# Optimization experiments

Hardware: AMD Instinct MI355X
Metric: run time of the kernel (lower is better)

## Reference

```python
import jax, jax.numpy as jnp
import numpy as np

B_SZ, T_LEN, M_DIM, S_DIM = 128, 8192, 64, 512
EPS = 1e-16  # stands in for config.R_epsilon / E_epsilon / l_epsilon


def setup_inputs() -> dict:
    key = jax.random.key(0)
    k1, k2, k3 = jax.random.split(key, 3)
    # one-hot encoded higher-order emission symbols, as the model feeds the cell
    sym = jax.random.randint(k1, (B_SZ, T_LEN), 0, M_DIM)
    x = jax.nn.one_hot(sym, M_DIM, dtype=jnp.float32)          # [B, T, M]
    # row-stochastic transition matrix (model.A(A_kernel) produces probabilities)
    A = jax.nn.softmax(jax.random.normal(k2, (S_DIM, S_DIM)), axis=1)
    # emission matrix: column s is the emission distribution of state s
    B = jax.nn.softmax(jax.random.normal(k3, (M_DIM, S_DIM)), axis=0)
    return {"x": x, "A": A, "B": B}


def _logsumexp_row(alpha):
    # calc_new_cell_state: log(sum(exp(alpha - m) + l_eps)) + m, over states
    m = jnp.max(alpha, axis=1, keepdims=True)
    return jnp.log(jnp.sum(jnp.exp(alpha - m) + EPS, axis=1, keepdims=True)) + m


def reference(x, A, B):
    bsz, T, M = x.shape
    S = A.shape[0]
    # E_t = x_t @ B for all t at once (same math as per-step get_E)
    E = jnp.einsum('btm,ms->bts', x, B)                         # [B, T, S]

    # get_initial_state: all probability mass on state 0
    init_fwd = jnp.concatenate(
        [jnp.ones((bsz, 1), x.dtype), jnp.zeros((bsz, S - 1), x.dtype)], axis=1)
    # first call has init=True: R = log(old_forward)
    R0 = jnp.log(init_fwd)                                      # [0, -inf, ...]
    alpha0 = jnp.log(E[:, 0] + EPS) + R0                        # [B, S]

    def step(alpha_prev, E_t):
        # get_R: max-subtract log-domain sparse/dense matmul trick
        m = jnp.max(alpha_prev, axis=1, keepdims=True)
        R = jnp.log(jnp.exp(alpha_prev - m) @ A + EPS) + m
        # calc_new_cell_state
        alpha = jnp.log(E_t + EPS) + R
        return alpha, None

    E_time_major = jnp.swapaxes(E, 0, 1)                        # [T, B, S]
    alpha_T, _ = jax.lax.scan(step, alpha0, E_time_major[1:])
    loglik = _logsumexp_row(alpha_T)                            # [B, 1]
    return alpha_T, loglik
```

## Files before the change

kernel.cpp:

```cpp
#include <hip/hip_runtime.h>
#include <stdint.h>

#define BSZ  128
#define TLEN 8192
#define MDIM 64
#define SDIM 512
#define NEG_BIG (-1e30f)
#define QA   127

typedef int i32x4 __attribute__((ext_vector_type(4)));

__device__ __forceinline__ float wave_max_f32(float x) {
  int v = __builtin_bit_cast(int, x);
#define DPP_STEP(ctrl)                                                        \
  {                                                                           \
    int o = __builtin_amdgcn_update_dpp(v, v, ctrl, 0xf, 0xf, false);         \
    v = __builtin_bit_cast(int, fmaxf(__builtin_bit_cast(float, v),           \
                                      __builtin_bit_cast(float, o)));         \
  }
  DPP_STEP(0x111)
  DPP_STEP(0x112)
  DPP_STEP(0x114)
  DPP_STEP(0x118)
  DPP_STEP(0x142)
  DPP_STEP(0x143)
#undef DPP_STEP
  return __builtin_bit_cast(float, __builtin_amdgcn_readlane(v, 63));
}

__global__ void sym_kernel(const float* __restrict__ x, uint8_t* __restrict__ sym) {
  int i = blockIdx.x * blockDim.x + threadIdx.x;
  const float4* p = (const float4*)(x + (size_t)i * MDIM);
  int idx = 0;
  #pragma unroll
  for (int j = 0; j < 16; ++j) {
    float4 v = p[j];
    if (v.x > 0.5f) idx = 4*j + 0;
    if (v.y > 0.5f) idx = 4*j + 1;
    if (v.z > 0.5f) idx = 4*j + 2;
    if (v.w > 0.5f) idx = 4*j + 3;
  }
  sym[i] = (uint8_t)idx;
}

__global__ void colmax_kernel(const float* __restrict__ A, float* __restrict__ cmax) {
  int c = blockIdx.x, l = threadIdx.x;
  float m = 0.f;
  for (int r = l; r < SDIM; r += 64) m = fmaxf(m, A[(size_t)r * SDIM + c]);
  #pragma unroll
  for (int off = 32; off; off >>= 1) m = fmaxf(m, __shfl_xor(m, off));
  if (l == 0) cmax[c] = m;
}

__global__ void pack_kernel(const float* __restrict__ A, const float* __restrict__ cmax,
                            unsigned* __restrict__ Aq) {
  int id = blockIdx.x * 256 + threadIdx.x;
  int c = id >> 7, j = id & 127;
  float s = (float)QA / cmax[c];
  unsigned q = 0;
  #pragma unroll
  for (int bb = 0; bb < 4; ++bb) {
    float v = A[(size_t)(4 * j + bb) * SDIM + c];
    int qi = (int)(v * s + 0.5f);
    if (qi > QA) qi = QA;
    q |= (unsigned)qi << (8 * bb);
  }
  Aq[c * 128 + j] = q;
}

__global__
#if __has_attribute(amdgpu_waves_per_eu)
__attribute__((amdgpu_waves_per_eu(2, 2)))
#endif
__launch_bounds__(512) void hmm_fwd(
    const unsigned* __restrict__ Aq, const float* __restrict__ cmax,
    const float* __restrict__ Bm, const uint8_t* __restrict__ sym,
    float* __restrict__ out) {
  const int b  = blockIdx.x;
  const int t  = threadIdx.x;
  const int wv = t >> 6;
  const int ln = t & 63;
  const int pg = ln >> 4;

  __shared__ __align__(16) uint8_t p8[SDIM];
  __shared__ float red[8];
  __shared__ float red2[8];

  const uint4* aq4 = (const uint4*)Aq;
  const int cb = (wv << 6) + (ln & 15);
#define LDB(TT, KT) aq4[(size_t)(cb + 16 * TT) * 32 + KT * 4 + pg]
  uint4 B00=LDB(0,0),B01=LDB(0,1),B02=LDB(0,2),B03=LDB(0,3),
        B04=LDB(0,4),B05=LDB(0,5),B06=LDB(0,6),B07=LDB(0,7);
  uint4 B10=LDB(1,0),B11=LDB(1,1),B12=LDB(1,2),B13=LDB(1,3),
        B14=LDB(1,4),B15=LDB(1,5),B16=LDB(1,6),B17=LDB(1,7);
  uint4 B20=LDB(2,0),B21=LDB(2,1),B22=LDB(2,2),B23=LDB(2,3),
        B24=LDB(2,4),B25=LDB(2,5),B26=LDB(2,6),B27=LDB(2,7);
  uint4 B30=LDB(3,0),B31=LDB(3,1),B32=LDB(3,2),B33=LDB(3,3),
        B34=LDB(3,4),B35=LDB(3,5),B36=LDB(3,6),B37=LDB(3,7);
#undef LDB

  const float cscale = cmax[t] * (1.0f / ((float)QA * (float)QA));
  const uint8_t* symb = sym + (size_t)b * TLEN;

  int s0 = symb[0];
  float vReg = (t == 0) ? (Bm[s0 * SDIM + t] + 1e-16f) : 0.f;
  int   E_acc = 0;
  int   symNext = symb[1];
  float Ecur = Bm[symNext * SDIM + t] + 1e-16f;
  symNext = symb[2];

  for (int step = 1; step < TLEN; ++step) {
    float m_w = wave_max_f32(vReg);
    if (ln == 0) red[wv] = m_w;
    float Enxt  = Bm[symNext * SDIM + t] + 1e-16f;
    int   symNN = (int)symb[(step + 2 <= TLEN - 1) ? step + 2 : TLEN - 1];
    __syncthreads();

    float4 ra = *(const float4*)&red[0];
    float4 rb = *(const float4*)&red[4];
    float gm = fmaxf(fmaxf(fmaxf(ra.x, ra.y), fmaxf(ra.z, ra.w)),
                     fmaxf(fmaxf(rb.x, rb.y), fmaxf(rb.z, rb.w)));
    unsigned eb = (__builtin_bit_cast(unsigned, gm) >> 23) & 255u;
    float sqQ = __builtin_bit_cast(float, (253u - eb) << 23) * (float)QA;
    unsigned q = (unsigned)fmaf(vReg, sqQ, 0.5f);
    p8[t] = (uint8_t)q;
    __syncthreads();

    const uint4* pq = (const uint4*)p8;
    uint4 P0 = pq[0*4+pg], P1 = pq[1*4+pg], P2 = pq[2*4+pg], P3 = pq[3*4+pg];
    uint4 P4 = pq[4*4+pg], P5 = pq[5*4+pg], P6 = pq[6*4+pg], P7 = pq[7*4+pg];

    i32x4 l0={0,0,0,0}, l1={0,0,0,0}, l2={0,0,0,0}, l3={0,0,0,0};
    i32x4 h0={0,0,0,0}, h1={0,0,0,0}, h2={0,0,0,0}, h3={0,0,0,0};
#define MF(P, B, C) C = __builtin_amdgcn_mfma_i32_16x16x64_i8(              \
        __builtin_bit_cast(i32x4, P), __builtin_bit_cast(i32x4, B), C, 0, 0, 0)
    MF(P0, B00, l0); MF(P0, B10, l1); MF(P0, B20, l2); MF(P0, B30, l3);
    MF(P4, B04, h0); MF(P4, B14, h1); MF(P4, B24, h2); MF(P4, B34, h3);
    MF(P1, B01, l0); MF(P1, B11, l1); MF(P1, B21, l2); MF(P1, B31, l3);
    MF(P5, B05, h0); MF(P5, B15, h1); MF(P5, B25, h2); MF(P5, B35, h3);
    MF(P2, B02, l0); MF(P2, B12, l1); MF(P2, B22, l2); MF(P2, B32, l3);
    MF(P6, B06, h0); MF(P6, B16, h1); MF(P6, B26, h2); MF(P6, B36, h3);
    MF(P3, B03, l0); MF(P3, B13, l1); MF(P3, B23, l2); MF(P3, B33, l3);
    MF(P7, B07, h0); MF(P7, B17, h1); MF(P7, B27, h2); MF(P7, B37, h3);
#undef MF

    int rlo = (pg & 2) ? ((pg & 1) ? l3.x : l2.x)
                       : ((pg & 1) ? l1.x : l0.x);
    int rhi = (pg & 2) ? ((pg & 1) ? h3.x : h2.x)
                       : ((pg & 1) ? h1.x : h0.x);
    int rv = rlo + rhi;

    vReg  = fmaf((float)rv, cscale, 1e-16f) * Ecur;
    E_acc += (int)eb - 126;
    Ecur  = Enxt;
    symNext = symNN;
  }

  float alphaReg = __logf(vReg) + (float)E_acc * 0.6931471805599453f;
  out[(size_t)b * SDIM + t] = alphaReg;

  float mx = wave_max_f32(alphaReg);
  if (ln == 0) red2[wv] = mx;
  __syncthreads();
  float mf = fmaxf(fmaxf(fmaxf(red2[0], red2[1]), fmaxf(red2[2], red2[3])),
                   fmaxf(fmaxf(red2[4], red2[5]), fmaxf(red2[6], red2[7])));

  float se = __expf(alphaReg - mf);
  #pragma unroll
  for (int off = 32; off; off >>= 1) se += __shfl_xor(se, off);
  __syncthreads();
  if (ln == 0) red2[wv] = se;
  __syncthreads();
  if (t == 0) {
    float tot = 0.f;
    #pragma unroll
    for (int k = 0; k < 8; ++k) tot += red2[k];
    out[(size_t)BSZ * SDIM + b] = __logf(tot + SDIM * 1e-16f) + mf;
  }
}

extern "C" void kernel_launch(void* const* d_in, const int* in_sizes, int n_in,
                              void* d_out, int out_size, void* d_ws, size_t ws_size,
                              hipStream_t stream) {
  const float* x  = (const float*)d_in[0];
  const float* A  = (const float*)d_in[1];
  const float* Bm = (const float*)d_in[2];
  float* out = (float*)d_out;

  uint8_t*  sym  = (uint8_t*)d_ws;
  unsigned* Aq   = (unsigned*)((char*)d_ws + (1 << 20));
  float*    cmax = (float*)((char*)d_ws + (1 << 20) + (256 << 10));

  sym_kernel<<<(BSZ * TLEN) / 256, 256, 0, stream>>>(x, sym);
  colmax_kernel<<<SDIM, 64, 0, stream>>>(A, cmax);
  pack_kernel<<<(SDIM * 128) / 256, 256, 0, stream>>>(A, cmax, Aq);
  hmm_fwd<<<BSZ, 512, 0, stream>>>(Aq, cmax, Bm, sym, out);
}
```

Before: 6.854 ms.

## Offload one quarter of output columns from MFMA to dot4 VALU path

Drops the fourth MFMA column tile and computes those 16 columns per wave with packed 8-bit dot4 instructions. The A data for that tile is reloaded from global memory every step, and the partial sums are reduced across lane groups with shuffles. The aim is to shorten the serial MFMA chain per step by running MFMA and VALU work in parallel. In exchange each step now does extra global loads, LDS reads and cross-lane shuffles.

Result: slower. 9.001 ms (+31.3%).

```diff
diff --git a/kernel.cpp b/kernel.cpp
--- a/kernel.cpp
+++ b/kernel.cpp
@@ -9,6 +9,24 @@
 #define QA   127
 
 typedef int i32x4 __attribute__((ext_vector_type(4)));
+
+#if __has_builtin(__builtin_amdgcn_udot4)
+  __device__ __forceinline__ int dot4(unsigned a, unsigned b, int c) {
+    return (int)__builtin_amdgcn_udot4(a, b, (unsigned)c, false);
+  }
+#elif __has_builtin(__builtin_amdgcn_sdot4)
+  __device__ __forceinline__ int dot4(unsigned a, unsigned b, int c) {
+    return __builtin_amdgcn_sdot4((int)a, (int)b, c, false);
+  }
+#else
+  __device__ __forceinline__ int dot4(unsigned a, unsigned b, int c) {
+    c += (int)((a & 0xffu) * (b & 0xffu));
+    c += (int)(((a >> 8) & 0xffu) * ((b >> 8) & 0xffu));
+    c += (int)(((a >> 16) & 0xffu) * ((b >> 16) & 0xffu));
+    c += (int)((a >> 24) * (b >> 24));
+    return c;
+  }
+#endif
 
 __device__ __forceinline__ float wave_max_f32(float x) {
   int v = __builtin_bit_cast(int, x);
@@ -95,9 +113,10 @@
         B14=LDB(1,4),B15=LDB(1,5),B16=LDB(1,6),B17=LDB(1,7);
   uint4 B20=LDB(2,0),B21=LDB(2,1),B22=LDB(2,2),B23=LDB(2,3),
         B24=LDB(2,4),B25=LDB(2,5),B26=LDB(2,6),B27=LDB(2,7);
-  uint4 B30=LDB(3,0),B31=LDB(3,1),B32=LDB(3,2),B33=LDB(3,3),
-        B34=LDB(3,4),B35=LDB(3,5),B36=LDB(3,6),B37=LDB(3,7);
 #undef LDB
+
+  const uint4* dA = (const uint4*)(Aq + (size_t)((wv << 6) + 48 + (ln & 15)) * 128
+                                   + (pg << 5));
 
   const float cscale = cmax[t] * (1.0f / ((float)QA * (float)QA));
   const uint8_t* symb = sym + (size_t)b * TLEN;
@@ -112,6 +131,8 @@
   for (int step = 1; step < TLEN; ++step) {
     float m_w = wave_max_f32(vReg);
     if (ln == 0) red[wv] = m_w;
+    uint4 A0 = dA[0], A1 = dA[1], A2 = dA[2], A3 = dA[3];
+    uint4 A4 = dA[4], A5 = dA[5], A6 = dA[6], A7 = dA[7];
     float Enxt  = Bm[symNext * SDIM + t] + 1e-16f;
     int   symNN = (int)symb[(step + 2 <= TLEN - 1) ? step + 2 : TLEN - 1];
     __syncthreads();
@@ -129,26 +150,37 @@
     const uint4* pq = (const uint4*)p8;
     uint4 P0 = pq[0*4+pg], P1 = pq[1*4+pg], P2 = pq[2*4+pg], P3 = pq[3*4+pg];
     uint4 P4 = pq[4*4+pg], P5 = pq[5*4+pg], P6 = pq[6*4+pg], P7 = pq[7*4+pg];
-
-    i32x4 l0={0,0,0,0}, l1={0,0,0,0}, l2={0,0,0,0}, l3={0,0,0,0};
-    i32x4 h0={0,0,0,0}, h1={0,0,0,0}, h2={0,0,0,0}, h3={0,0,0,0};
+    const uint4* pd = (const uint4*)(p8 + (pg << 7));
+    uint4 D0 = pd[0], D1 = pd[1], D2 = pd[2], D3 = pd[3];
+    uint4 D4 = pd[4], D5 = pd[5], D6 = pd[6], D7 = pd[7];
+
+    i32x4 l0={0,0,0,0}, l1={0,0,0,0}, l2={0,0,0,0};
+    i32x4 h0={0,0,0,0}, h1={0,0,0,0}, h2={0,0,0,0};
 #define MF(P, B, C) C = __builtin_amdgcn_mfma_i32_16x16x64_i8(              \
         __builtin_bit_cast(i32x4, P), __builtin_bit_cast(i32x4, B), C, 0, 0, 0)
-    MF(P0, B00, l0); MF(P0, B10, l1); MF(P0, B20, l2); MF(P0, B30, l3);
-    MF(P4, B04, h0); MF(P4, B14, h1); MF(P4, B24, h2); MF(P4, B34, h3);
-    MF(P1, B01, l0); MF(P1, B11, l1); MF(P1, B21, l2); MF(P1, B31, l3);
-    MF(P5, B05, h0); MF(P5, B15, h1); MF(P5, B25, h2); MF(P5, B35, h3);
-    MF(P2, B02, l0); MF(P2, B12, l1); MF(P2, B22, l2); MF(P2, B32, l3);
-    MF(P6, B06, h0); MF(P6, B16, h1); MF(P6, B26, h2); MF(P6, B36, h3);
-    MF(P3, B03, l0); MF(P3, B13, l1); MF(P3, B23, l2); MF(P3, B33, l3);
-    MF(P7, B07, h0); MF(P7, B17, h1); MF(P7, B27, h2); MF(P7, B37, h3);
+    MF(P0, B00, l0); MF(P0, B10, l1); MF(P0, B20, l2);
+    MF(P1, B01, l0); MF(P1, B11, l1); MF(P1, B21, l2);
+    MF(P2, B02, l0); MF(P2, B12, l1); MF(P2, B22, l2);
+    MF(P3, B03, l0); MF(P3, B13, l1); MF(P3, B23, l2);
+    MF(P4, B04, h0); MF(P4, B14, h1); MF(P4, B24, h2);
+    MF(P5, B05, h0); MF(P5, B15, h1); MF(P5, B25, h2);
+    MF(P6, B06, h0); MF(P6, B16, h1); MF(P6, B26, h2);
+    MF(P7, B07, h0); MF(P7, B17, h1); MF(P7, B27, h2);
 #undef MF
 
-    int rlo = (pg & 2) ? ((pg & 1) ? l3.x : l2.x)
-                       : ((pg & 1) ? l1.x : l0.x);
-    int rhi = (pg & 2) ? ((pg & 1) ? h3.x : h2.x)
-                       : ((pg & 1) ? h1.x : h0.x);
-    int rv = rlo + rhi;
+    int d = 0;
+#define DD(PV, AV)                                                            \
+    d = dot4(PV.x, AV.x, d); d = dot4(PV.y, AV.y, d);                         \
+    d = dot4(PV.z, AV.z, d); d = dot4(PV.w, AV.w, d);
+    DD(D0, A0) DD(D1, A1) DD(D2, A2) DD(D3, A3)
+    DD(D4, A4) DD(D5, A5) DD(D6, A6) DD(D7, A7)
+#undef DD
+    d += __shfl_xor(d, 16);
+    d += __shfl_xor(d, 32);
+
+    int rlo = (pg == 0) ? l0.x : (pg == 1) ? l1.x : l2.x;
+    int rhi = (pg == 0) ? h0.x : (pg == 1) ? h1.x : h2.x;
+    int rv  = (pg == 3) ? d : (rlo + rhi);
 
     vReg  = fmaf((float)rv, cscale, 1e-16f) * Ecur;
     E_acc += (int)eb - 126;
```

## Quantize per wave with local exponent, drop one barrier per step

Applied to the files above, without the earlier changes.

Each wave now quantizes its 64 probabilities to int8 using its own max exponent and publishes that exponent to shared memory, so each step needs one barrier instead of two. The shared buffers are double-buffered by step parity to avoid write-after-read races. After the barrier, every K-block's bytes are shifted right by the exponent difference to the global maximum, and blocks more than 6 exponents below are skipped entirely. This adds per-block integer shift/mask work and can lose precision through the extra rounding.

New measurement: 9.046 ms. 32.0% more time.

```diff
diff --git a/kernel.cpp b/kernel.cpp
--- a/kernel.cpp
+++ b/kernel.cpp
@@ -82,8 +82,8 @@
   const int ln = t & 63;
   const int pg = ln >> 4;
 
-  __shared__ __align__(16) uint8_t p8[SDIM];
-  __shared__ float red[8];
+  __shared__ __align__(16) uint8_t p8[2][SDIM];
+  __shared__ __align__(8)  uint8_t e8[2][8];
   __shared__ float red2[8];
 
   const uint4* aq4 = (const uint4*)Aq;
@@ -110,38 +110,58 @@
   symNext = symb[2];
 
   for (int step = 1; step < TLEN; ++step) {
+    const int par = step & 1;
+
     float m_w = wave_max_f32(vReg);
-    if (ln == 0) red[wv] = m_w;
+    unsigned ebw = (__builtin_bit_cast(unsigned, m_w) >> 23) & 255u;
+    float sqQ = __builtin_bit_cast(float, (253u - ebw) << 23) * (float)QA;
+    p8[par][t] = (uint8_t)(unsigned)fmaf(vReg, sqQ, 0.5f);
+    if (ln == 0) e8[par][wv] = (uint8_t)ebw;
+    __syncthreads();
+
     float Enxt  = Bm[symNext * SDIM + t] + 1e-16f;
     int   symNN = (int)symb[(step + 2 <= TLEN - 1) ? step + 2 : TLEN - 1];
-    __syncthreads();
-
-    float4 ra = *(const float4*)&red[0];
-    float4 rb = *(const float4*)&red[4];
-    float gm = fmaxf(fmaxf(fmaxf(ra.x, ra.y), fmaxf(ra.z, ra.w)),
-                     fmaxf(fmaxf(rb.x, rb.y), fmaxf(rb.z, rb.w)));
-    unsigned eb = (__builtin_bit_cast(unsigned, gm) >> 23) & 255u;
-    float sqQ = __builtin_bit_cast(float, (253u - eb) << 23) * (float)QA;
-    unsigned q = (unsigned)fmaf(vReg, sqQ, 0.5f);
-    p8[t] = (uint8_t)q;
-    __syncthreads();
-
-    const uint4* pq = (const uint4*)p8;
+
+    uint2 ev = *(const uint2*)&e8[par][0];
+    unsigned sx = (unsigned)__builtin_amdgcn_readfirstlane((int)ev.x);
+    unsigned sy = (unsigned)__builtin_amdgcn_readfirstlane((int)ev.y);
+    unsigned ek0 = sx & 255u, ek1 = (sx >> 8) & 255u,
+             ek2 = (sx >> 16) & 255u, ek3 = sx >> 24;
+    unsigned ek4 = sy & 255u, ek5 = (sy >> 8) & 255u,
+             ek6 = (sy >> 16) & 255u, ek7 = sy >> 24;
+    unsigned Ea = ek0 > ek1 ? ek0 : ek1, Eb = ek2 > ek3 ? ek2 : ek3;
+    unsigned Ec = ek4 > ek5 ? ek4 : ek5, Ed = ek6 > ek7 ? ek6 : ek7;
+    unsigned Ee = Ea > Eb ? Ea : Eb,     Ef = Ec > Ed ? Ec : Ed;
+    unsigned E  = Ee > Ef ? Ee : Ef;
+
+    const uint4* pq = (const uint4*)p8[par];
     uint4 P0 = pq[0*4+pg], P1 = pq[1*4+pg], P2 = pq[2*4+pg], P3 = pq[3*4+pg];
     uint4 P4 = pq[4*4+pg], P5 = pq[5*4+pg], P6 = pq[6*4+pg], P7 = pq[7*4+pg];
 
     i32x4 l0={0,0,0,0}, l1={0,0,0,0}, l2={0,0,0,0}, l3={0,0,0,0};
     i32x4 h0={0,0,0,0}, h1={0,0,0,0}, h2={0,0,0,0}, h3={0,0,0,0};
-#define MF(P, B, C) C = __builtin_amdgcn_mfma_i32_16x16x64_i8(              \
+#define MF(P, B, C) C = __builtin_amdgcn_mfma_i32_16x16x64_i8(                \
         __builtin_bit_cast(i32x4, P), __builtin_bit_cast(i32x4, B), C, 0, 0, 0)
-    MF(P0, B00, l0); MF(P0, B10, l1); MF(P0, B20, l2); MF(P0, B30, l3);
-    MF(P4, B04, h0); MF(P4, B14, h1); MF(P4, B24, h2); MF(P4, B34, h3);
-    MF(P1, B01, l0); MF(P1, B11, l1); MF(P1, B21, l2); MF(P1, B31, l3);
-    MF(P5, B05, h0); MF(P5, B15, h1); MF(P5, B25, h2); MF(P5, B35, h3);
-    MF(P2, B02, l0); MF(P2, B12, l1); MF(P2, B22, l2); MF(P2, B32, l3);
-    MF(P6, B06, h0); MF(P6, B16, h1); MF(P6, B26, h2); MF(P6, B36, h3);
-    MF(P3, B03, l0); MF(P3, B13, l1); MF(P3, B23, l2); MF(P3, B33, l3);
-    MF(P7, B07, h0); MF(P7, B17, h1); MF(P7, B27, h2); MF(P7, B37, h3);
+#define KT_BLOCK(PK, EK, C0, C1, C2, C3, BT0, BT1, BT2, BT3)                  \
+    {                                                                         \
+      unsigned d = E - (EK);                                                  \
+      if (d < 7u) {                                                           \
+        unsigned rb = d ? 0x01010101u * (1u << (d - 1)) : 0u;                 \
+        unsigned mk = (0xFFu >> d) * 0x01010101u;                             \
+        PK.x = ((PK.x + rb) >> d) & mk; PK.y = ((PK.y + rb) >> d) & mk;       \
+        PK.z = ((PK.z + rb) >> d) & mk; PK.w = ((PK.w + rb) >> d) & mk;       \
+        MF(PK, BT0, C0); MF(PK, BT1, C1); MF(PK, BT2, C2); MF(PK, BT3, C3);   \
+      }                                                                       \
+    }
+    KT_BLOCK(P0, ek0, l0, l1, l2, l3, B00, B10, B20, B30)
+    KT_BLOCK(P1, ek1, l0, l1, l2, l3, B01, B11, B21, B31)
+    KT_BLOCK(P2, ek2, l0, l1, l2, l3, B02, B12, B22, B32)
+    KT_BLOCK(P3, ek3, l0, l1, l2, l3, B03, B13, B23, B33)
+    KT_BLOCK(P4, ek4, h0, h1, h2, h3, B04, B14, B24, B34)
+    KT_BLOCK(P5, ek5, h0, h1, h2, h3, B05, B15, B25, B35)
+    KT_BLOCK(P6, ek6, h0, h1, h2, h3, B06, B16, B26, B36)
+    KT_BLOCK(P7, ek7, h0, h1, h2, h3, B07, B17, B27, B37)
+#undef KT_BLOCK
 #undef MF
 
     int rlo = (pg & 2) ? ((pg & 1) ? l3.x : l2.x)
@@ -151,7 +171,7 @@
     int rv = rlo + rhi;
 
     vReg  = fmaf((float)rv, cscale, 1e-16f) * Ecur;
-    E_acc += (int)eb - 126;
+    E_acc += (int)E - 126;
     Ecur  = Enxt;
     symNext = symNN;
   }
```

## Split per-block recurrence across 16 waves with half the MFMA work each

Applied to the files above, without the earlier changes.

Doubles the block to 1024 threads so each wave computes only 32 output states per timestep with 16 int8 MFMAs instead of 64 states with 32. The aim is to shorten the per-step serial MFMA chain and halve the register footprint of the preloaded quantized transition matrix. Half of each wave's lanes become redundant duplicates, masked on writes, and the per-step block barriers and max reduction now span 16 waves.

Result: slower. 8.148 ms (+18.9%).

```diff
diff --git a/kernel.cpp b/kernel.cpp
--- a/kernel.cpp
+++ b/kernel.cpp
@@ -70,85 +70,84 @@
 
 __global__
 #if __has_attribute(amdgpu_waves_per_eu)
-__attribute__((amdgpu_waves_per_eu(2, 2)))
+__attribute__((amdgpu_waves_per_eu(4, 4)))
 #endif
-__launch_bounds__(512) void hmm_fwd(
+__launch_bounds__(1024) void hmm_fwd(
     const unsigned* __restrict__ Aq, const float* __restrict__ cmax,
     const float* __restrict__ Bm, const uint8_t* __restrict__ sym,
     float* __restrict__ out) {
-  const int b  = blockIdx.x;
-  const int t  = threadIdx.x;
-  const int wv = t >> 6;
-  const int ln = t & 63;
-  const int pg = ln >> 4;
+  const int b   = blockIdx.x;
+  const int t   = threadIdx.x;
+  const int w   = t >> 6;
+  const int ln  = t & 63;
+  const int pg  = ln >> 4;
+  const int sel = pg & 1;
+  const int c   = (w << 5) + (sel << 4) + (ln & 15);
+  const bool act = (ln < 32);
 
   __shared__ __align__(16) uint8_t p8[SDIM];
-  __shared__ float red[8];
-  __shared__ float red2[8];
+  __shared__ float red[16];
+  __shared__ float red2[16];
 
   const uint4* aq4 = (const uint4*)Aq;
-  const int cb = (wv << 6) + (ln & 15);
-#define LDB(TT, KT) aq4[(size_t)(cb + 16 * TT) * 32 + KT * 4 + pg]
+  const int cbase = (w << 5) + (ln & 15);
+#define LDB(TT, KT) aq4[(size_t)(cbase + 16 * TT) * 32 + KT * 4 + pg]
   uint4 B00=LDB(0,0),B01=LDB(0,1),B02=LDB(0,2),B03=LDB(0,3),
         B04=LDB(0,4),B05=LDB(0,5),B06=LDB(0,6),B07=LDB(0,7);
   uint4 B10=LDB(1,0),B11=LDB(1,1),B12=LDB(1,2),B13=LDB(1,3),
         B14=LDB(1,4),B15=LDB(1,5),B16=LDB(1,6),B17=LDB(1,7);
-  uint4 B20=LDB(2,0),B21=LDB(2,1),B22=LDB(2,2),B23=LDB(2,3),
-        B24=LDB(2,4),B25=LDB(2,5),B26=LDB(2,6),B27=LDB(2,7);
-  uint4 B30=LDB(3,0),B31=LDB(3,1),B32=LDB(3,2),B33=LDB(3,3),
-        B34=LDB(3,4),B35=LDB(3,5),B36=LDB(3,6),B37=LDB(3,7);
 #undef LDB
 
-  const float cscale = cmax[t] * (1.0f / ((float)QA * (float)QA));
+  const float cscale = cmax[c] * (1.0f / ((float)QA * (float)QA));
   const uint8_t* symb = sym + (size_t)b * TLEN;
 
   int s0 = symb[0];
-  float vReg = (t == 0) ? (Bm[s0 * SDIM + t] + 1e-16f) : 0.f;
+  float vReg = (c == 0) ? (Bm[s0 * SDIM + c] + 1e-16f) : 0.f;
   int   E_acc = 0;
   int   symNext = symb[1];
-  float Ecur = Bm[symNext * SDIM + t] + 1e-16f;
+  float Ecur = Bm[symNext * SDIM + c] + 1e-16f;
   symNext = symb[2];
 
   for (int step = 1; step < TLEN; ++step) {
     float m_w = wave_max_f32(vReg);
-    if (ln == 0) red[wv] = m_w;
-    float Enxt  = Bm[symNext * SDIM + t] + 1e-16f;
+    if (ln == 0) red[w] = m_w;
+    float Enxt  = Bm[symNext * SDIM + c] + 1e-16f;
     int   symNN = (int)symb[(step + 2 <= TLEN - 1) ? step + 2 : TLEN - 1];
     __syncthreads();
 
-    float4 ra = *(const float4*)&red[0];
-    float4 rb = *(const float4*)&red[4];
-    float gm = fmaxf(fmaxf(fmaxf(ra.x, ra.y), fmaxf(ra.z, ra.w)),
-                     fmaxf(fmaxf(rb.x, rb.y), fmaxf(rb.z, rb.w)));
+    float4 r0 = *(const float4*)&red[0];
+    float4 r1 = *(const float4*)&red[4];
+    float4 r2 = *(const float4*)&red[8];
+    float4 r3 = *(const float4*)&red[12];
+    float g0 = fmaxf(fmaxf(r0.x, r0.y), fmaxf(r0.z, r0.w));
+    float g1 = fmaxf(fmaxf(r1.x, r1.y), fmaxf(r1.z, r1.w));
+    float g2 = fmaxf(fmaxf(r2.x, r2.y), fmaxf(r2.z, r2.w));
+    float g3 = fmaxf(fmaxf(r3.x, r3.y), fmaxf(r3.z, r3.w));
+    float gm = fmaxf(fmaxf(g0, g1), fmaxf(g2, g3));
     unsigned eb = (__builtin_bit_cast(unsigned, gm) >> 23) & 255u;
     float sqQ = __builtin_bit_cast(float, (253u - eb) << 23) * (float)QA;
     unsigned q = (unsigned)fmaf(vReg, sqQ, 0.5f);
-    p8[t] = (uint8_t)q;
+    if (act) p8[c] = (uint8_t)q;
     __syncthreads();
 
     const uint4* pq = (const uint4*)p8;
     uint4 P0 = pq[0*4+pg], P1 = pq[1*4+pg], P2 = pq[2*4+pg], P3 = pq[3*4+pg];
-    uint4 P4 = pq[4*4+pg], P5 = pq[5*4+pg], P6 = pq[6*4+pg], P7 = pq[7*4+pg];
-
-    i32x4 l0={0,0,0,0}, l1={0,0,0,0}, l2={0,0,0,0}, l3={0,0,0,0};
-    i32x4 h0={0,0,0,0}, h1={0,0,0,0}, h2={0,0,0,0}, h3={0,0,0,0};
+
+    i32x4 l0={0,0,0,0}, l1={0,0,0,0}, h0={0,0,0,0}, h1={0,0,0,0};
 #define MF(P, B, C) C = __builtin_amdgcn_mfma_i32_16x16x64_i8(              \
         __builtin_bit_cast(i32x4, P), __builtin_bit_cast(i32x4, B), C, 0, 0, 0)
-    MF(P0, B00, l0); MF(P0, B10, l1); MF(P0, B20, l2); MF(P0, B30, l3);
-    MF(P4, B04, h0); MF(P4, B14, h1); MF(P4, B24, h2); MF(P4, B34, h3);
-    MF(P1, B01, l0); MF(P1, B11, l1); MF(P1, B21, l2); MF(P1, B31, l3);
-    MF(P5, B05, h0); MF(P5, B15, h1); MF(P5, B25, h2); MF(P5, B35, h3);
-    MF(P2, B02, l0); MF(P2, B12, l1); MF(P2, B22, l2); MF(P2, B32, l3);
-    MF(P6, B06, h0); MF(P6, B16, h1); MF(P6, B26, h2); MF(P6, B36, h3);
-    MF(P3, B03, l0); MF(P3, B13, l1); MF(P3, B23, l2); MF(P3, B33, l3);
-    MF(P7, B07, h0); MF(P7, B17, h1); MF(P7, B27, h2); MF(P7, B37, h3);
+    MF(P0, B00, l0); MF(P0, B10, l1);
+    MF(P1, B01, l0); MF(P1, B11, l1);
+    MF(P2, B02, l0); MF(P2, B12, l1);
+    MF(P3, B03, l0); MF(P3, B13, l1);
+    uint4 P4 = pq[4*4+pg], P5 = pq[5*4+pg], P6 = pq[6*4+pg], P7 = pq[7*4+pg];
+    MF(P4, B04, h0); MF(P4, B14, h1);
+    MF(P5, B05, h0); MF(P5, B15, h1);
+    MF(P6, B06, h0); MF(P6, B16, h1);
+    MF(P7, B07, h0); MF(P7, B17, h1);
 #undef MF
 
-    int rlo = (pg & 2) ? ((pg & 1) ? l3.x : l2.x)
-                       : ((pg & 1) ? l1.x : l0.x);
-    int rhi = (pg & 2) ? ((pg & 1) ? h3.x : h2.x)
-                       : ((pg & 1) ? h1.x : h0.x);
-    int rv = rlo + rhi;
+    int rv = sel ? (l1.x + h1.x) : (l0.x + h0.x);
 
     vReg  = fmaf((float)rv, cscale, 1e-16f) * Ecur;
     E_acc += (int)eb - 126;
@@ -157,24 +156,31 @@
   }
 
   float alphaReg = __logf(vReg) + (float)E_acc * 0.6931471805599453f;
-  out[(size_t)b * SDIM + t] = alphaReg;
+  if (act) out[(size_t)b * SDIM + c] = alphaReg;
 
   float mx = wave_max_f32(alphaReg);
-  if (ln == 0) red2[wv] = mx;
+  if (ln == 0) red2[w] = mx;
   __syncthreads();
-  float mf = fmaxf(fmaxf(fmaxf(red2[0], red2[1]), fmaxf(red2[2], red2[3])),
-                   fmaxf(fmaxf(red2[4], red2[5]), fmaxf(red2[6], red2[7])));
-
-  float se = __expf(alphaReg - mf);
+  float4 q0 = *(const float4*)&red2[0];
+  float4 q1 = *(const float4*)&red2[4];
+  float4 q2 = *(const float4*)&red2[8];
+  float4 q3 = *(const float4*)&red2[12];
+  float mf = fmaxf(
+      fmaxf(fmaxf(fmaxf(q0.x, q0.y), fmaxf(q0.z, q0.w)),
+            fmaxf(fmaxf(q1.x, q1.y), fmaxf(q1.z, q1.w))),
+      fmaxf(fmaxf(fmaxf(q2.x, q2.y), fmaxf(q2.z, q2.w)),
+            fmaxf(fmaxf(q3.x, q3.y), fmaxf(q3.z, q3.w))));
+
+  float se = act ? __expf(alphaReg - mf) : 0.f;
   #pragma unroll
   for (int off = 32; off; off >>= 1) se += __shfl_xor(se, off);
   __syncthreads();
-  if (ln == 0) red2[wv] = se;
+  if (ln == 0) red2[w] = se;
   __syncthreads();
   if (t == 0) {
     float tot = 0.f;
     #pragma unroll
-    for (int k = 0; k < 8; ++k) tot += red2[k];
+    for (int k = 0; k < 16; ++k) tot += red2[k];
     out[(size_t)BSZ * SDIM + b] = __logf(tot + SDIM * 1e-16f) + mf;
   }
 }
@@ -194,5 +200,5 @@
   sym_kernel<<<(BSZ * TLEN) / 256, 256, 0, stream>>>(x, sym);
   colmax_kernel<<<SDIM, 64, 0, stream>>>(A, cmax);
   pack_kernel<<<(SDIM * 128) / 256, 256, 0, stream>>>(A, cmax, Aq);
-  hmm_fwd<<<BSZ, 512, 0, stream>>>(Aq, cmax, Bm, sym, out);
-}
+  hmm_fwd<<<BSZ, 1024, 0, stream>>>(Aq, cmax, Bm, sym, out);
+}
```
